# Kernel optimization log

Measured on AMD Instinct MI355X. Metric: run time of the kernel, lower is better.

## Reference

```python
import jax, jax.numpy as jnp
import numpy as np

EPS = 1e-5

def layer_norm(x, g, b):
    m = jnp.mean(x, axis=-1, keepdims=True)
    v = jnp.var(x, axis=-1, keepdims=True)
    return (x - m) / jnp.sqrt(v + EPS) * g + b

def setup_inputs() -> dict:
    key = jax.random.key(0)
    B, N, D, H, F = 2, 2048, 1024, 16, 4096
    ks = jax.random.split(key, 12)
    s = 0.02
    return {
        "x": jax.random.normal(ks[0], (B, N, D), dtype=jnp.float32),
        "wq": jax.random.normal(ks[1], (D, D), dtype=jnp.float32) * s,
        "bq": jnp.zeros((D,), jnp.float32),
        "wk": jax.random.normal(ks[2], (D, D), dtype=jnp.float32) * s,
        "bk": jnp.zeros((D,), jnp.float32),
        "wv": jax.random.normal(ks[3], (D, D), dtype=jnp.float32) * s,
        "bv": jnp.zeros((D,), jnp.float32),
        "g1": jnp.ones((D,), jnp.float32),
        "b1": jnp.zeros((D,), jnp.float32),
        "g2": jnp.ones((D,), jnp.float32),
        "b2": jnp.zeros((D,), jnp.float32),
        "w1": jax.random.normal(ks[4], (D, F), dtype=jnp.float32) * s,
        "bw1": jnp.zeros((F,), jnp.float32),
        "gf": jnp.ones((F,), jnp.float32),
        "bf": jnp.zeros((F,), jnp.float32),
        "w2": jax.random.normal(ks[5], (F, D), dtype=jnp.float32) * s,
        "bw2": jnp.zeros((D,), jnp.float32),
        "num_heads": 16,
    }

def reference(x, wq, bq, wk, bk, wv, bv, g1, b1, g2, b2, w1, bw1, gf, bf, w2, bw2, num_heads):
    B, N, D = x.shape
    H = num_heads
    E = D // H
    h = layer_norm(x, g1, b1)
    q = (h @ wq + bq).reshape(B, N, H, E).transpose(0, 2, 1, 3)  # B H N E
    k = (h @ wk + bk).reshape(B, N, H, E).transpose(0, 2, 1, 3)
    v = (h @ wv + bv).reshape(B, N, H, E).transpose(0, 2, 1, 3)
    # NOTE: original scales by 1/sqrt(1/emb_dim) == sqrt(emb_dim)
    scale = jnp.sqrt(jnp.float32(D))
    score = jnp.einsum('bhne,bhme->bhnm', q, k) * scale  # B H N N
    w = jax.nn.softmax(score, axis=-1)
    attn = jnp.einsum('bhnm,bhme->bhne', w, v)
    attn = attn.transpose(0, 2, 1, 3).reshape(B, N, D)
    x = x + attn  # dropout = identity in eval
    h2 = layer_norm(x, g2, b2)
    # MLP: Linear -> (Dropout) -> LayerNorm -> ReLU -> Linear; NO residual add (faithful to source)
    u = layer_norm(h2 @ w1 + bw1, gf, bf)
    return jax.nn.relu(u) @ w2 + bw2
```

## Files before the change

kernel.cpp:

```cpp
#include <hip/hip_runtime.h>

typedef unsigned short u16;
typedef _Float16 f16;
typedef _Float16 f16x8 __attribute__((ext_vector_type(8)));
typedef float f32x4 __attribute__((ext_vector_type(4)));
typedef unsigned short u16x4 __attribute__((ext_vector_type(4)));
typedef unsigned int u32x4 __attribute__((ext_vector_type(4)));

__device__ __forceinline__ u16 f2h(float f) {
    f16 h = (f16)f;
    return *reinterpret_cast<u16*>(&h);
}
__device__ __forceinline__ float h2f(u16 u) {
    f16 h = *reinterpret_cast<f16*>(&u);
    return (float)h;
}

__device__ __forceinline__ float exp2v(float x) { return __builtin_amdgcn_exp2f(x); }

__device__ __forceinline__ unsigned cvtpkh(float lo, float hi) {
    unsigned r;
    asm("v_cvt_pkrtz_f16_f32 %0, %1, %2" : "=v"(r) : "v"(lo), "v"(hi));
    return r;
}

__device__ __forceinline__ void gload16(const u16* g, u16* l) {
    __builtin_amdgcn_global_load_lds((const __attribute__((address_space(1))) unsigned int*)g,
                                     (__attribute__((address_space(3))) unsigned int*)l, 16, 0, 0);
}

#define RAW_BARRIER() __builtin_amdgcn_s_barrier()
#define WAITCNT_VM(N) asm volatile("s_waitcnt vmcnt(" #N ")" ::: "memory")

__device__ __forceinline__ int xcd_swz(int bid, int nwg) {
    return (bid & 7) * (nwg >> 3) + (bid >> 3);
}

__global__ void transpose_cast3(const float* __restrict__ W0, u16* __restrict__ T0,
                                const float* __restrict__ W1, u16* __restrict__ T1,
                                const float* __restrict__ W2, u16* __restrict__ T2,
                                int K, int N) {
    __shared__ float t[32][33];
    const float* W = (blockIdx.z == 0) ? W0 : (blockIdx.z == 1) ? W1 : W2;
    u16* Wt = (blockIdx.z == 0) ? T0 : (blockIdx.z == 1) ? T1 : T2;
    const int n0 = blockIdx.x * 32, k0 = blockIdx.y * 32;
    const int tx = threadIdx.x, ty = threadIdx.y;
#pragma unroll
    for (int i = 0; i < 32; i += 8)
        t[ty + i][tx] = W[(size_t)(k0 + ty + i) * N + n0 + tx];
    __syncthreads();
#pragma unroll
    for (int i = 0; i < 32; i += 8)
        Wt[(size_t)(n0 + ty + i) * K + k0 + tx] = f2h(t[tx][ty + i]);
}

__global__ void transpose_cast(const float* __restrict__ W, u16* __restrict__ Wt,
                               int K, int N) {
    __shared__ float t[32][33];
    const int n0 = blockIdx.x * 32, k0 = blockIdx.y * 32;
    const int tx = threadIdx.x, ty = threadIdx.y;
#pragma unroll
    for (int i = 0; i < 32; i += 8)
        t[ty + i][tx] = W[(size_t)(k0 + ty + i) * N + n0 + tx];
    __syncthreads();
#pragma unroll
    for (int i = 0; i < 32; i += 8)
        Wt[(size_t)(n0 + ty + i) * K + k0 + tx] = f2h(t[tx][ty + i]);
}

__global__ __launch_bounds__(256) void ln_f32_f16(const float* __restrict__ in,
                                                  const float* __restrict__ g,
                                                  const float* __restrict__ b,
                                                  u16* __restrict__ out) {
    constexpr int Dl = 1024;
    const int row = blockIdx.x, tid = threadIdx.x;
    const float4 v = *(const float4*)&in[(size_t)row * Dl + tid * 4];
    const float* vp = (const float*)&v;
    float s = v.x + v.y + v.z + v.w;
    float s2 = v.x * v.x + v.y * v.y + v.z * v.z + v.w * v.w;
#pragma unroll
    for (int off = 32; off; off >>= 1) { s += __shfl_xor(s, off); s2 += __shfl_xor(s2, off); }
    __shared__ float red[8];
    const int lane = tid & 63, wid = tid >> 6;
    if (lane == 0) { red[wid] = s; red[4 + wid] = s2; }
    __syncthreads();
    s = red[0] + red[1] + red[2] + red[3];
    s2 = red[4] + red[5] + red[6] + red[7];
    const float mean = s * (1.0f / Dl);
    const float rstd = rsqrtf(s2 * (1.0f / Dl) - mean * mean + 1e-5f);
    u16x4 pk;
#pragma unroll
    for (int i = 0; i < 4; ++i) {
        const int col = tid * 4 + i;
        pk[i] = f2h((vp[i] - mean) * rstd * g[col] + b[col]);
    }
    *(u16x4*)&out[(size_t)row * Dl + tid * 4] = pk;
}

__global__ __launch_bounds__(256) void ln_relu_f16(u16* __restrict__ mid,
                                                   const float* __restrict__ g,
                                                   const float* __restrict__ b) {
    constexpr int Fl = 4096;
    const int row = blockIdx.x, tid = threadIdx.x;
    u16* rp = mid + (size_t)row * Fl;
    float v[16];
    u32x4 raw[2];
#pragma unroll
    for (int c = 0; c < 2; ++c) raw[c] = *(const u32x4*)&rp[tid * 16 + c * 8];
#pragma unroll
    for (int c = 0; c < 2; ++c)
#pragma unroll
        for (int j = 0; j < 4; ++j) {
            const unsigned u = raw[c][j];
            v[c * 8 + j * 2] = h2f((u16)(u & 0xffffu));
            v[c * 8 + j * 2 + 1] = h2f((u16)(u >> 16));
        }
    float s = 0.f, s2 = 0.f;
#pragma unroll
    for (int i = 0; i < 16; ++i) { s += v[i]; s2 += v[i] * v[i]; }
#pragma unroll
    for (int off = 32; off; off >>= 1) { s += __shfl_xor(s, off); s2 += __shfl_xor(s2, off); }
    __shared__ float red[8];
    const int lane = tid & 63, wid = tid >> 6;
    if (lane == 0) { red[wid] = s; red[4 + wid] = s2; }
    __syncthreads();
    s = red[0] + red[1] + red[2] + red[3];
    s2 = red[4] + red[5] + red[6] + red[7];
    const float mean = s * (1.0f / Fl);
    const float rstd = rsqrtf(s2 * (1.0f / Fl) - mean * mean + 1e-5f);
    unsigned w[8];
#pragma unroll
    for (int j = 0; j < 8; ++j) {
        const int col = tid * 16 + j * 2;
        const float y0 = fmaxf((v[j * 2] - mean) * rstd * g[col] + b[col], 0.f);
        const float y1 = fmaxf((v[j * 2 + 1] - mean) * rstd * g[col + 1] + b[col + 1], 0.f);
        w[j] = (unsigned)f2h(y0) | ((unsigned)f2h(y1) << 16);
    }
    *(u32x4*)&rp[tid * 16] = *(u32x4*)&w[0];
    *(u32x4*)&rp[tid * 16 + 8] = *(u32x4*)&w[4];
}

template <int EPI, int BN>
__global__ __launch_bounds__(256, 2) void gemm_f16(const u16* __restrict__ A,
                                                   const u16* __restrict__ Bt,
                                                   const float* __restrict__ bias,
                                                   u16* __restrict__ outB,
                                                   float* __restrict__ outF,
                                                   int M_, int N_, int K_) {
    constexpr int BK = 32;
    constexpr int NJ = BN / 32;
    __shared__ u16 As[2][128 * BK];
    __shared__ u16 Bs[2][BN * BK];
    const int tid = threadIdx.x;
    const int lane = tid & 63;
    const int wid = tid >> 6;
    const int swz = xcd_swz(blockIdx.y * gridDim.x + blockIdx.x, gridDim.x * gridDim.y);
    const int m0 = (swz / gridDim.x) * 128;
    const int n0 = (swz % gridDim.x) * BN;
    const int wr = (wid >> 1) * 64;
    const int wc = (wid & 1) * (BN / 2);
    const int fr = lane & 15;
    const int fg = (lane >> 4) * 8;

    const int srow = wid * 32 + (lane >> 2);
    const int srB = wid * (BN / 4) + (lane >> 2);
    const int scol = (lane & 3) * 8;
    const u16* pa0 = A + (size_t)(m0 + srow) * K_ + scol;
    const u16* pa1 = pa0 + (size_t)16 * K_;
    const u16* pb0 = Bt + (size_t)(n0 + srB) * K_ + scol;
    const u16* pb1 = pb0 + (size_t)16 * K_;
    const int aoff = wid * 1024;
    const int boff = wid * (BN / 4) * BK;

    auto stage = [&](int k0, int buf) {
        gload16(pa0 + k0, &As[buf][aoff]);
        gload16(pa1 + k0, &As[buf][aoff + 512]);
        gload16(pb0 + k0, &Bs[buf][boff]);
        if constexpr (BN == 128) gload16(pb1 + k0, &Bs[buf][boff + 512]);
    };

    f32x4 acc[4][NJ] = {};
    const int nt = K_ / BK;

    stage(0, 0);
    WAITCNT_VM(0);
    RAW_BARRIER();

    for (int t = 0; t < nt; ++t) {
        const int buf = t & 1;
        if (t + 1 < nt) stage((t + 1) * BK, buf ^ 1);
        f16x8 aF[4], bF[NJ];
#pragma unroll
        for (int i = 0; i < 4; ++i) aF[i] = *(const f16x8*)&As[buf][(wr + i * 16 + fr) * BK + fg];
#pragma unroll
        for (int j = 0; j < NJ; ++j) bF[j] = *(const f16x8*)&Bs[buf][(wc + j * 16 + fr) * BK + fg];
#pragma unroll
        for (int i = 0; i < 4; ++i)
#pragma unroll
            for (int j = 0; j < NJ; ++j)
                acc[i][j] = __builtin_amdgcn_mfma_f32_16x16x32_f16(aF[i], bF[j], acc[i][j], 0, 0, 0);
        WAITCNT_VM(0);
        RAW_BARRIER();
    }

    const int g4 = (lane >> 4) * 4;
#pragma unroll
    for (int i = 0; i < 4; ++i) {
#pragma unroll
        for (int j = 0; j < NJ; ++j) {
            const int mb = m0 + wr + i * 16 + g4;
            const int nb = n0 + wc + j * 16 + fr;
            const float bv = bias[nb];
            if constexpr (EPI == 0) {
#pragma unroll
                for (int r = 0; r < 4; ++r)
                    outB[(size_t)(mb + r) * N_ + nb] = f2h(acc[i][j][r] + bv);
            } else {
#pragma unroll
                for (int r = 0; r < 4; ++r)
                    outF[(size_t)(mb + r) * N_ + nb] = acc[i][j][r] + bv;
            }
        }
    }
}

__global__ __launch_bounds__(256, 4) void gemm_qkv(const u16* __restrict__ A,
                                                   const u16* __restrict__ qW,
                                                   const u16* __restrict__ kW,
                                                   const u16* __restrict__ vW,
                                                   const float* __restrict__ bq,
                                                   const float* __restrict__ bk,
                                                   const float* __restrict__ bv,
                                                   u16* __restrict__ qb, u16* __restrict__ kb,
                                                   u16* __restrict__ vtb,
                                                   int M_, int K_) {
    constexpr int BK = 32;
    __shared__ u16 As[2][128 * BK];
    __shared__ u16 Bs[2][64 * BK];
    const int tid = threadIdx.x;
    const int lane = tid & 63;
    const int wid = tid >> 6;
    const int swz = xcd_swz(blockIdx.y * gridDim.x + blockIdx.x, gridDim.x * gridDim.y);
    const int bx = swz % gridDim.x;
    const int region = bx >> 4;
    const int n0 = (bx & 15) * 64;
    const int m0 = (swz / gridDim.x) * 128;
    const int wr = (wid >> 1) * 64;
    const int wc = (wid & 1) * 32;
    const int fr = lane & 15;
    const int fg = (lane >> 4) * 8;

    const int srow = wid * 32 + (lane >> 2);
    const int srB = wid * 16 + (lane >> 2);
    const int scol = (lane & 3) * 8;

    const u16* B = (region == 0) ? qW : (region == 1) ? kW : vW;
    const u16* pa0 = A + (size_t)(m0 + srow) * K_ + scol;
    const u16* pa1 = pa0 + (size_t)16 * K_;
    const u16* pb = B + (size_t)(n0 + srB) * K_ + scol;
    const int aoff = wid * 1024;
    const int boff = wid * 512;

    auto stage = [&](int k0, int buf) {
        gload16(pa0 + k0, &As[buf][aoff]);
        gload16(pa1 + k0, &As[buf][aoff + 512]);
        gload16(pb + k0, &Bs[buf][boff]);
    };

    f32x4 acc[4][2] = {};
    const int nt = K_ / BK;

    stage(0, 0);
    WAITCNT_VM(0);
    RAW_BARRIER();

    for (int t = 0; t < nt; ++t) {
        const int buf = t & 1;
        if (t + 1 < nt) stage((t + 1) * BK, buf ^ 1);
        f16x8 aF[4], bF[2];
#pragma unroll
        for (int i = 0; i < 4; ++i) aF[i] = *(const f16x8*)&As[buf][(wr + i * 16 + fr) * BK + fg];
#pragma unroll
        for (int j = 0; j < 2; ++j) bF[j] = *(const f16x8*)&Bs[buf][(wc + j * 16 + fr) * BK + fg];
#pragma unroll
        for (int i = 0; i < 4; ++i)
#pragma unroll
            for (int j = 0; j < 2; ++j)
                acc[i][j] = __builtin_amdgcn_mfma_f32_16x16x32_f16(aF[i], bF[j], acc[i][j], 0, 0, 0);
        WAITCNT_VM(0);
        RAW_BARRIER();
    }

    const float* bias = (region == 0) ? bq : (region == 1) ? bk : bv;
    const float scale = (region == 0) ? 32.f : 1.f;
    const int g4 = (lane >> 4) * 4;
#pragma unroll
    for (int i = 0; i < 4; ++i) {
#pragma unroll
        for (int j = 0; j < 2; ++j) {
            const int mb = m0 + wr + i * 16 + g4;
            const int nb = n0 + wc + j * 16 + fr;
            const float bv_ = bias[nb];
            const int h = nb >> 6, e = nb & 63;
            if (region < 2) {
                u16* outp = (region == 0) ? qb : kb;
#pragma unroll
                for (int r = 0; r < 4; ++r) {
                    const int m = mb + r;
                    const size_t idx = ((size_t)((m >> 11) * 16 + h) * 2048 + (m & 2047)) * 64 + e;
                    outp[idx] = f2h((acc[i][j][r] + bv_) * scale);
                }
            } else {
                const int b_ = mb >> 11, np = mb & 2047;
                u16x4 pk;
#pragma unroll
                for (int r = 0; r < 4; ++r) pk[r] = f2h(acc[i][j][r] + bv_);
                *(u16x4*)&vtb[((size_t)(b_ * 16 + h) * 64 + e) * 2048 + np] = pk;
            }
        }
    }
}

__global__ __launch_bounds__(512, 4) void attn_kernel(const u16* __restrict__ q,
                                                      const u16* __restrict__ k,
                                                      const u16* __restrict__ vt,
                                                      const float* __restrict__ x,
                                                      float* __restrict__ x2) {
    constexpr int N = 2048, E = 64, KB = 64, NT = N / KB;
    constexpr float L2E = 1.4426950408889634f;
    __shared__ u16 Ks[2][64 * 64];
    __shared__ u16 Vs[2][64 * 64];
    __shared__ unsigned Ps[8][16][36];

    const int tid = threadIdx.x;
    const int lane = tid & 63;
    const int wid = tid >> 6;
    const int swzb = xcd_swz(blockIdx.x, gridDim.x);
    const int bh = swzb >> 4;
    const int q0 = (swzb & 15) * 128;
    const u16* qh = q + (size_t)bh * N * E;
    const u16* kh = k + (size_t)bh * N * E;
    const u16* vh = vt + (size_t)bh * E * N;

    const int fr = lane & 15;
    const int fgrp = lane >> 4;
    const int fg8 = fgrp * 8;
    int pc[2];
#pragma unroll
    for (int ks = 0; ks < 2; ++ks) pc[ks] = 8 * (((ks << 2) + fgrp) ^ (fr & 7));

    const int srow = wid * 8 + (lane >> 3);
    const int swc = 8 * ((lane & 7) ^ (lane >> 3));
    u16* dK = &Ks[0][wid * 8 * 64];
    u16* dV = &Vs[0][wid * 8 * 64];
    constexpr int BUFO = 64 * 64;

    f16x8 qf[2];
#pragma unroll
    for (int ks = 0; ks < 2; ++ks)
        qf[ks] = *(const f16x8*)&qh[(size_t)(q0 + wid * 16 + fr) * E + ks * 32 + fg8];

    auto stage = [&](int t, int buf) {
        const size_t kb = (size_t)t * KB;
        gload16(kh + (kb + srow) * E + swc, dK + buf * BUFO);
        gload16(vh + (size_t)srow * N + kb + swc, dV + buf * BUFO);
    };

    f32x4 o[4] = {};
    float mrow = -1e30f, lpart = 0.f;

    stage(0, 0);

    for (int t = 0; t < NT; ++t) {
        const int buf = t & 1;
        RAW_BARRIER();
        if (t + 1 < NT) {
            stage(t + 1, buf ^ 1);
            WAITCNT_VM(2);
        } else {
            WAITCNT_VM(0);
        }
        RAW_BARRIER();

        const u16* KK = &Ks[buf][0];
        const u16* VV = &Vs[buf][0];

        f32x4 s[4] = {};
        __builtin_amdgcn_s_setprio(1);
#pragma unroll
        for (int fn = 0; fn < 4; ++fn)
#pragma unroll
            for (int ks = 0; ks < 2; ++ks) {
                const f16x8 kf = *(const f16x8*)&KK[(fn * 16 + fr) * 64 + pc[ks]];
                s[fn] = __builtin_amdgcn_mfma_f32_16x16x32_f16(kf, qf[ks], s[fn], 0, 0, 0);
            }
        __builtin_amdgcn_s_setprio(0);

        float lmax = fmaxf(fmaxf(fmaxf(s[0][0], s[0][1]), fmaxf(s[0][2], s[0][3])),
                           fmaxf(fmaxf(s[1][0], s[1][1]), fmaxf(s[1][2], s[1][3])));
        lmax = fmaxf(lmax, fmaxf(fmaxf(fmaxf(s[2][0], s[2][1]), fmaxf(s[2][2], s[2][3])),
                                 fmaxf(fmaxf(s[3][0], s[3][1]), fmaxf(s[3][2], s[3][3]))));
        if (!__all(lmax <= mrow + 8.f)) {
            float m2 = fmaxf(lmax, __shfl_xor(lmax, 16));
            m2 = fmaxf(m2, __shfl_xor(m2, 32));
            const float mnew = fmaxf(mrow, m2);
            const float fac = exp2v((mrow - mnew) * L2E);
            mrow = mnew;
            lpart *= fac;
            float fo[4];
#pragma unroll
            for (int r = 0; r < 4; ++r) fo[r] = __shfl(fac, fgrp * 4 + r);
#pragma unroll
            for (int fe = 0; fe < 4; ++fe)
#pragma unroll
                for (int r = 0; r < 4; ++r) o[fe][r] *= fo[r];
        }

        const float nml = -mrow * L2E;
#pragma unroll
        for (int fn = 0; fn < 4; ++fn) {
            const float p0 = exp2v(fmaf(s[fn][0], L2E, nml));
            const float p1 = exp2v(fmaf(s[fn][1], L2E, nml));
            const float p2 = exp2v(fmaf(s[fn][2], L2E, nml));
            const float p3 = exp2v(fmaf(s[fn][3], L2E, nml));
            lpart += (p0 + p1) + (p2 + p3);
            uint2 w;
            w.x = cvtpkh(p0, p1);
            w.y = cvtpkh(p2, p3);
            *(uint2*)&Ps[wid][fr][fn * 8 + fgrp * 2] = w;
        }

        const u16* prow = (const u16*)&Ps[wid][fr][0];
        f16x8 pf[2];
#pragma unroll
        for (int ks = 0; ks < 2; ++ks) pf[ks] = *(const f16x8*)&prow[ks * 32 + fg8];
        __builtin_amdgcn_s_setprio(1);
#pragma unroll
        for (int fe = 0; fe < 4; ++fe)
#pragma unroll
            for (int ks = 0; ks < 2; ++ks) {
                const f16x8 vf = *(const f16x8*)&VV[(fe * 16 + fr) * 64 + pc[ks]];
                o[fe] = __builtin_amdgcn_mfma_f32_16x16x32_f16(pf[ks], vf, o[fe], 0, 0, 0);
            }
        __builtin_amdgcn_s_setprio(0);
    }

    float lsum = lpart + __shfl_xor(lpart, 16);
    lsum += __shfl_xor(lsum, 32);
    float rl[4];
#pragma unroll
    for (int r = 0; r < 4; ++r) rl[r] = 1.0f / __shfl(lsum, fgrp * 4 + r);

    const int b_ = bh >> 4, h_ = bh & 15;
#pragma unroll
    for (int fe = 0; fe < 4; ++fe)
#pragma unroll
        for (int r = 0; r < 4; ++r) {
            const int npos = q0 + wid * 16 + fgrp * 4 + r;
            const size_t idx = ((size_t)(b_ * 2048 + npos)) * 1024 + h_ * 64 + fe * 16 + fr;
            x2[idx] = x[idx] + o[fe][r] * rl[r];
        }
}

extern "C" void kernel_launch(void* const* d_in, const int* in_sizes, int n_in,
                              void* d_out, int out_size, void* d_ws, size_t ws_size,
                              hipStream_t stream) {
    const float* x = (const float*)d_in[0];
    const float* wq = (const float*)d_in[1];
    const float* bq = (const float*)d_in[2];
    const float* wk = (const float*)d_in[3];
    const float* bk = (const float*)d_in[4];
    const float* wv = (const float*)d_in[5];
    const float* bv = (const float*)d_in[6];
    const float* g1 = (const float*)d_in[7];
    const float* b1 = (const float*)d_in[8];
    const float* g2 = (const float*)d_in[9];
    const float* b2 = (const float*)d_in[10];
    const float* w1 = (const float*)d_in[11];
    const float* bw1 = (const float*)d_in[12];
    const float* gf = (const float*)d_in[13];
    const float* bf = (const float*)d_in[14];
    const float* w2 = (const float*)d_in[15];
    const float* bw2 = (const float*)d_in[16];
    float* out = (float*)d_out;

    constexpr int Bc = 2, Nc = 2048, Dc = 1024, Fc = 4096, Mc = 4096;

    char* ws = (char*)d_ws;
    auto alloc = [&](size_t bytes) {
        char* p = ws;
        ws += (bytes + 255) & ~(size_t)255;
        return p;
    };
    u16* wqt = (u16*)alloc((size_t)Dc * Dc * 2);
    u16* wkt = (u16*)alloc((size_t)Dc * Dc * 2);
    u16* wvt = (u16*)alloc((size_t)Dc * Dc * 2);
    u16* w1t = (u16*)alloc((size_t)Dc * Fc * 2);
    u16* w2t = (u16*)alloc((size_t)Fc * Dc * 2);
    char* region = (char*)alloc((size_t)Mc * Dc * 2 * 4);
    u16* h1 = (u16*)region;
    u16* qb = h1 + (size_t)Mc * Dc;
    u16* kb = qb + (size_t)Mc * Dc;
    u16* vtb = kb + (size_t)Mc * Dc;
    u16* mid = (u16*)region;
    float* x2 = (float*)alloc((size_t)Mc * Dc * 4);
    u16* h2 = (u16*)alloc((size_t)Mc * Dc * 2);

    const dim3 tb(32, 8);
    transpose_cast3<<<dim3(Dc / 32, Dc / 32, 3), tb, 0, stream>>>(wq, wqt, wk, wkt, wv, wvt, Dc, Dc);
    transpose_cast<<<dim3(Fc / 32, Dc / 32), tb, 0, stream>>>(w1, w1t, Dc, Fc);
    transpose_cast<<<dim3(Dc / 32, Fc / 32), tb, 0, stream>>>(w2, w2t, Fc, Dc);

    ln_f32_f16<<<Mc, 256, 0, stream>>>(x, g1, b1, h1);

    gemm_qkv<<<dim3(48, Mc / 128), 256, 0, stream>>>(h1, wqt, wkt, wvt, bq, bk, bv,
                                                     qb, kb, vtb, Mc, Dc);

    attn_kernel<<<Bc * 16 * (Nc / 128), 512, 0, stream>>>(qb, kb, vtb, x, x2);

    ln_f32_f16<<<Mc, 256, 0, stream>>>(x2, g2, b2, h2);

    gemm_f16<0, 128><<<dim3(Fc / 128, Mc / 128), 256, 0, stream>>>(h2, w1t, bw1, mid, nullptr, Mc, Fc, Dc);

    ln_relu_f16<<<Mc, 256, 0, stream>>>(mid, gf, bf);

    gemm_f16<1, 64><<<dim3(Dc / 64, Mc / 128), 256, 0, stream>>>(mid, w2t, bw2, nullptr, out, Mc, Dc, Fc);
}
```

Before: 263.8 us.

## Triple-buffer LDS in GEMM kernels with partial vmcnt waits

Both the generic GEMM and the fused QKV GEMM move from double to triple-buffered shared memory, prefetching two K-tiles ahead. Partial vmcnt waits replace the full drain each iteration, so global loads for later tiles stay in flight while the current tile is consumed by MFMAs. The change adds LDS use per block and lowers the QKV kernel's launch-bounds occupancy hint from 4 to 2. The wait counts assume a fixed number of load instructions per stage, so they must match what the compiler emits.

Result: slower. 274.8 us (+4.2%).

```diff
diff --git a/kernel.cpp b/kernel.cpp
--- a/kernel.cpp
+++ b/kernel.cpp
@@ -149,8 +149,8 @@
                                                    int M_, int N_, int K_) {
     constexpr int BK = 32;
     constexpr int NJ = BN / 32;
-    __shared__ u16 As[2][128 * BK];
-    __shared__ u16 Bs[2][BN * BK];
+    __shared__ u16 As[3][128 * BK];
+    __shared__ u16 Bs[3][BN * BK];
     const int tid = threadIdx.x;
     const int lane = tid & 63;
     const int wid = tid >> 6;
@@ -183,24 +183,31 @@
     const int nt = K_ / BK;
 
     stage(0, 0);
-    WAITCNT_VM(0);
-    RAW_BARRIER();
+    stage(BK, 1);
+    int cur = 0, nx1 = 1, nx2 = 2;
 
     for (int t = 0; t < nt; ++t) {
-        const int buf = t & 1;
-        if (t + 1 < nt) stage((t + 1) * BK, buf ^ 1);
+        if (t + 2 < nt) {
+            stage((t + 2) * BK, nx2);
+            if constexpr (BN == 128) { WAITCNT_VM(8); } else { WAITCNT_VM(6); }
+        } else if (t + 1 < nt) {
+            if constexpr (BN == 128) { WAITCNT_VM(4); } else { WAITCNT_VM(3); }
+        } else {
+            WAITCNT_VM(0);
+        }
+        RAW_BARRIER();
         f16x8 aF[4], bF[NJ];
 #pragma unroll
-        for (int i = 0; i < 4; ++i) aF[i] = *(const f16x8*)&As[buf][(wr + i * 16 + fr) * BK + fg];
-#pragma unroll
-        for (int j = 0; j < NJ; ++j) bF[j] = *(const f16x8*)&Bs[buf][(wc + j * 16 + fr) * BK + fg];
+        for (int i = 0; i < 4; ++i) aF[i] = *(const f16x8*)&As[cur][(wr + i * 16 + fr) * BK + fg];
+#pragma unroll
+        for (int j = 0; j < NJ; ++j) bF[j] = *(const f16x8*)&Bs[cur][(wc + j * 16 + fr) * BK + fg];
 #pragma unroll
         for (int i = 0; i < 4; ++i)
 #pragma unroll
             for (int j = 0; j < NJ; ++j)
                 acc[i][j] = __builtin_amdgcn_mfma_f32_16x16x32_f16(aF[i], bF[j], acc[i][j], 0, 0, 0);
-        WAITCNT_VM(0);
         RAW_BARRIER();
+        const int tmp = cur; cur = nx1; nx1 = nx2; nx2 = tmp;
     }
 
     const int g4 = (lane >> 4) * 4;
@@ -224,7 +231,7 @@
     }
 }
 
-__global__ __launch_bounds__(256, 4) void gemm_qkv(const u16* __restrict__ A,
+__global__ __launch_bounds__(256, 2) void gemm_qkv(const u16* __restrict__ A,
                                                    const u16* __restrict__ qW,
                                                    const u16* __restrict__ kW,
                                                    const u16* __restrict__ vW,
@@ -235,8 +242,8 @@
                                                    u16* __restrict__ vtb,
                                                    int M_, int K_) {
     constexpr int BK = 32;
-    __shared__ u16 As[2][128 * BK];
-    __shared__ u16 Bs[2][64 * BK];
+    __shared__ u16 As[3][128 * BK];
+    __shared__ u16 Bs[3][64 * BK];
     const int tid = threadIdx.x;
     const int lane = tid & 63;
     const int wid = tid >> 6;
@@ -271,24 +278,31 @@
     const int nt = K_ / BK;
 
     stage(0, 0);
-    WAITCNT_VM(0);
-    RAW_BARRIER();
+    stage(BK, 1);
+    int cur = 0, nx1 = 1, nx2 = 2;
 
     for (int t = 0; t < nt; ++t) {
-        const int buf = t & 1;
-        if (t + 1 < nt) stage((t + 1) * BK, buf ^ 1);
+        if (t + 2 < nt) {
+            stage((t + 2) * BK, nx2);
+            WAITCNT_VM(6);
+        } else if (t + 1 < nt) {
+            WAITCNT_VM(3);
+        } else {
+            WAITCNT_VM(0);
+        }
+        RAW_BARRIER();
         f16x8 aF[4], bF[2];
 #pragma unroll
-        for (int i = 0; i < 4; ++i) aF[i] = *(const f16x8*)&As[buf][(wr + i * 16 + fr) * BK + fg];
-#pragma unroll
-        for (int j = 0; j < 2; ++j) bF[j] = *(const f16x8*)&Bs[buf][(wc + j * 16 + fr) * BK + fg];
+        for (int i = 0; i < 4; ++i) aF[i] = *(const f16x8*)&As[cur][(wr + i * 16 + fr) * BK + fg];
+#pragma unroll
+        for (int j = 0; j < 2; ++j) bF[j] = *(const f16x8*)&Bs[cur][(wc + j * 16 + fr) * BK + fg];
 #pragma unroll
         for (int i = 0; i < 4; ++i)
 #pragma unroll
             for (int j = 0; j < 2; ++j)
                 acc[i][j] = __builtin_amdgcn_mfma_f32_16x16x32_f16(aF[i], bF[j], acc[i][j], 0, 0, 0);
-        WAITCNT_VM(0);
         RAW_BARRIER();
+        const int tmp = cur; cur = nx1; nx1 = nx2; nx2 = tmp;
     }
 
     const float* bias = (region == 0) ? bq : (region == 1) ? bk : bv;
```

## Split-K the final MLP GEMM and reorder tile mapping M-major

Applied to the files above, without the earlier changes.

Replaces the final FFN down-projection GEMM (K=4096, only 512 blocks of 128x64) with a two-way split-K kernel that writes fp32 partials, followed by a small reduction kernel that adds the partials and the bias. The goal is more blocks in flight and shorter per-block K loops, so the GPU is better occupied. The block swizzle in the QKV and main GEMMs also changes from N-major to M-major tile order, which changes L2 reuse of weight versus activation tiles. The cost is an extra fp32 partial buffer write and read plus one more kernel launch.

Result: no change. 261.8 us (-0.7%).

```diff
diff --git a/kernel.cpp b/kernel.cpp
--- a/kernel.cpp
+++ b/kernel.cpp
@@ -154,9 +154,10 @@
     const int tid = threadIdx.x;
     const int lane = tid & 63;
     const int wid = tid >> 6;
+    const int nM = gridDim.y;
     const int swz = xcd_swz(blockIdx.y * gridDim.x + blockIdx.x, gridDim.x * gridDim.y);
-    const int m0 = (swz / gridDim.x) * 128;
-    const int n0 = (swz % gridDim.x) * BN;
+    const int m0 = (swz % nM) * 128;
+    const int n0 = (swz / nM) * BN;
     const int wr = (wid >> 1) * 64;
     const int wc = (wid & 1) * (BN / 2);
     const int fr = lane & 15;
@@ -211,17 +212,103 @@
             const int mb = m0 + wr + i * 16 + g4;
             const int nb = n0 + wc + j * 16 + fr;
             const float bv = bias[nb];
-            if constexpr (EPI == 0) {
-#pragma unroll
-                for (int r = 0; r < 4; ++r)
-                    outB[(size_t)(mb + r) * N_ + nb] = f2h(acc[i][j][r] + bv);
-            } else {
-#pragma unroll
-                for (int r = 0; r < 4; ++r)
-                    outF[(size_t)(mb + r) * N_ + nb] = acc[i][j][r] + bv;
-            }
-        }
-    }
+#pragma unroll
+            for (int r = 0; r < 4; ++r)
+                outB[(size_t)(mb + r) * N_ + nb] = f2h(acc[i][j][r] + bv);
+        }
+    }
+}
+
+__global__ __launch_bounds__(256, 4) void gemm_f16_splitk(const u16* __restrict__ A,
+                                                          const u16* __restrict__ Bt,
+                                                          float* __restrict__ p0,
+                                                          float* __restrict__ p1,
+                                                          int M_, int N_, int K_) {
+    constexpr int BK = 32, BN = 64;
+    __shared__ u16 As[2][128 * BK];
+    __shared__ u16 Bs[2][BN * BK];
+    const int tid = threadIdx.x;
+    const int lane = tid & 63;
+    const int wid = tid >> 6;
+    const int nM = gridDim.y;
+    const int swz = xcd_swz(blockIdx.y * gridDim.x + blockIdx.x, gridDim.x * gridDim.y);
+    const int m0 = (swz % nM) * 128;
+    const int n0 = (swz / nM) * BN;
+    const int kBase = blockIdx.z * (K_ >> 1);
+    float* dst = blockIdx.z ? p1 : p0;
+    const int wr = (wid >> 1) * 64;
+    const int wc = (wid & 1) * (BN / 2);
+    const int fr = lane & 15;
+    const int fg = (lane >> 4) * 8;
+
+    const int srow = wid * 32 + (lane >> 2);
+    const int srB = wid * (BN / 4) + (lane >> 2);
+    const int scol = (lane & 3) * 8;
+    const u16* pa0 = A + (size_t)(m0 + srow) * K_ + kBase + scol;
+    const u16* pa1 = pa0 + (size_t)16 * K_;
+    const u16* pb0 = Bt + (size_t)(n0 + srB) * K_ + kBase + scol;
+    const u16* pb1 = pb0 + (size_t)16 * K_;
+    const int aoff = wid * 1024;
+    const int boff = wid * (BN / 4) * BK;
+
+    auto stage = [&](int k0, int buf) {
+        gload16(pa0 + k0, &As[buf][aoff]);
+        gload16(pa1 + k0, &As[buf][aoff + 512]);
+        gload16(pb0 + k0, &Bs[buf][boff]);
+    };
+
+    f32x4 acc[4][2] = {};
+    const int nt = (K_ >> 1) / BK;
+
+    stage(0, 0);
+    WAITCNT_VM(0);
+    RAW_BARRIER();
+
+    for (int t = 0; t < nt; ++t) {
+        const int buf = t & 1;
+        if (t + 1 < nt) stage((t + 1) * BK, buf ^ 1);
+        f16x8 aF[4], bF[2];
+#pragma unroll
+        for (int i = 0; i < 4; ++i) aF[i] = *(const f16x8*)&As[buf][(wr + i * 16 + fr) * BK + fg];
+#pragma unroll
+        for (int j = 0; j < 2; ++j) bF[j] = *(const f16x8*)&Bs[buf][(wc + j * 16 + fr) * BK + fg];
+#pragma unroll
+        for (int i = 0; i < 4; ++i)
+#pragma unroll
+            for (int j = 0; j < 2; ++j)
+                acc[i][j] = __builtin_amdgcn_mfma_f32_16x16x32_f16(aF[i], bF[j], acc[i][j], 0, 0, 0);
+        WAITCNT_VM(0);
+        RAW_BARRIER();
+    }
+
+    const int g4 = (lane >> 4) * 4;
+#pragma unroll
+    for (int i = 0; i < 4; ++i)
+#pragma unroll
+        for (int j = 0; j < 2; ++j) {
+            const int mb = m0 + wr + i * 16 + g4;
+            const int nb = n0 + wc + j * 16 + fr;
+#pragma unroll
+            for (int r = 0; r < 4; ++r)
+                dst[(size_t)(mb + r) * N_ + nb] = acc[i][j][r];
+        }
+}
+
+__global__ __launch_bounds__(256) void reduce2_bias(const float* __restrict__ p0,
+                                                    const float* __restrict__ p1,
+                                                    const float* __restrict__ bias,
+                                                    float* __restrict__ out, int N_) {
+    const size_t i4 = (size_t)blockIdx.x * 256 + threadIdx.x;
+    const float4 a = ((const float4*)p0)[i4];
+    const float4 b = ((const float4*)p1)[i4];
+    const int col4 = (int)(i4 % (N_ / 4));
+    const float4 bi = ((const float4*)bias)[col4];
+    float4 o;
+    o.x = a.x + b.x + bi.x;
+    o.y = a.y + b.y + bi.y;
+    o.z = a.z + b.z + bi.z;
+    o.w = a.w + b.w + bi.w;
+    ((float4*)out)[i4] = o;
 }
 
 __global__ __launch_bounds__(256, 4) void gemm_qkv(const u16* __restrict__ A,
@@ -240,11 +327,12 @@
     const int tid = threadIdx.x;
     const int lane = tid & 63;
     const int wid = tid >> 6;
+    const int nM = gridDim.y;
     const int swz = xcd_swz(blockIdx.y * gridDim.x + blockIdx.x, gridDim.x * gridDim.y);
-    const int bx = swz % gridDim.x;
+    const int m0 = (swz % nM) * 128;
+    const int bx = swz / nM;
     const int region = bx >> 4;
     const int n0 = (bx & 15) * 64;
-    const int m0 = (swz / gridDim.x) * 128;
     const int wr = (wid >> 1) * 64;
     const int wc = (wid & 1) * 32;
     const int fr = lane & 15;
@@ -505,6 +593,8 @@
     u16* mid = (u16*)region;
     float* x2 = (float*)alloc((size_t)Mc * Dc * 4);
     u16* h2 = (u16*)alloc((size_t)Mc * Dc * 2);
+    float* p1 = (float*)alloc((size_t)Mc * Dc * 4);
+    float* p0 = x2;
 
     const dim3 tb(32, 8);
     transpose_cast3<<<dim3(Dc / 32, Dc / 32, 3), tb, 0, stream>>>(wq, wqt, wk, wkt, wv, wvt, Dc, Dc);
@@ -524,5 +614,6 @@
 
     ln_relu_f16<<<Mc, 256, 0, stream>>>(mid, gf, bf);
 
-    gemm_f16<1, 64><<<dim3(Dc / 64, Mc / 128), 256, 0, stream>>>(mid, w2t, bw2, nullptr, out, Mc, Dc, Fc);
-}
+    gemm_f16_splitk<<<dim3(Dc / 64, Mc / 128, 2), 256, 0, stream>>>(mid, w2t, p0, p1, Mc, Dc, Fc);
+    reduce2_bias<<<(Mc * Dc) / 1024, 256, 0, stream>>>(p0, p1, bw2, out, Dc);
+}
```
